# Performance work log

Measured on AMD Instinct MI355X. Metric: run time of the kernel, lower is better.

The kernel has to match this reference:

```python
import jax, jax.numpy as jnp
import numpy as np

EPS = 1e-6

def _layernorm(x):
    mu = jnp.mean(x, axis=-1, keepdims=True)
    var = jnp.mean(jnp.square(x - mu), axis=-1, keepdims=True)
    return (x - mu) / jnp.sqrt(var + EPS)

def setup_inputs() -> dict:
    key = jax.random.key(0)
    ks = jax.random.split(key, 12)
    B, N, C = 4, 1024, 1024
    H = 16
    Dff = 4 * C
    s = 0.02
    x = jax.random.normal(ks[0], (B, N, C), dtype=jnp.float32)
    mask = jax.random.randint(ks[1], (N, N), 0, 2) > 0  # True = attend
    wq = jax.random.normal(ks[2], (C, C), dtype=jnp.float32) * s
    bq = jnp.zeros((C,), dtype=jnp.float32)
    wkv = jax.random.normal(ks[3], (C, 2 * C), dtype=jnp.float32) * s
    bkv = jnp.zeros((2 * C,), dtype=jnp.float32)
    wo = jax.random.normal(ks[4], (C, C), dtype=jnp.float32) * s
    bo = jnp.zeros((C,), dtype=jnp.float32)
    w1 = jax.random.normal(ks[5], (C, Dff), dtype=jnp.float32) * s
    b1 = jnp.zeros((Dff,), dtype=jnp.float32)
    w2 = jax.random.normal(ks[6], (Dff, C), dtype=jnp.float32) * s
    b2 = jnp.zeros((C,), dtype=jnp.float32)
    return {"x": x, "mask": mask, "wq": wq, "bq": bq, "wkv": wkv, "bkv": bkv,
            "wo": wo, "bo": bo, "w1": w1, "b1": b1, "w2": w2, "b2": b2}

def reference(x, mask, wq, bq, wkv, bkv, wo, bo, w1, b1, w2, b2):
    B, N, C = x.shape
    H = 16
    d = C // H
    scale = d ** -0.5
    max_neg = -jnp.finfo(x.dtype).max
    # attn_bias: 0 where mask True, -max where False; broadcast [1,1,N,N]
    attn_bias = jnp.where(mask, jnp.asarray(0.0, x.dtype), jnp.asarray(max_neg, x.dtype))[None, None]

    # --- pre-norm attention ---
    xn = _layernorm(x)
    q = (xn @ wq + bq).reshape(B, N, H, d)
    kv = xn @ wkv + bkv
    k, v = jnp.split(kv, 2, axis=-1)
    k = k.reshape(B, N, H, d)
    v = v.reshape(B, N, H, d)
    sim = jnp.einsum('bihd,bjhd->bhij', q, k) * scale + attn_bias
    attn = jax.nn.softmax(sim, axis=-1)
    o = jnp.einsum('bhij,bjhd->bihd', attn, v).reshape(B, N, C)
    x = x + (o @ wo + bo)

    # --- pre-norm MLP with tanh-approx GELU ---
    xn = _layernorm(x)
    h = jax.nn.gelu(xn @ w1 + b1, approximate=True)
    x = x + (h @ w2 + b2)
    return x
```

## Files before the change

### kernel.cpp

```cpp
#include <hip/hip_runtime.h>
#include <hip/hip_bf16.h>

typedef short bf16x8 __attribute__((ext_vector_type(8)));
typedef float f32x4 __attribute__((ext_vector_type(4)));
typedef unsigned short u16x8 __attribute__((ext_vector_type(8)));

#define MFMA16(a,b,c) __builtin_amdgcn_mfma_f32_16x16x32_bf16((a),(b),(c),0,0,0)

__device__ inline unsigned short f32_to_bf16(float f){
  union { float f; unsigned u; } v; v.f = f;
  unsigned u = v.u;
  u += 0x7FFFu + ((u >> 16) & 1u);
  return (unsigned short)(u >> 16);
}
__device__ inline float bf16_to_f32(unsigned short u){
  union { unsigned u; float f; } v; v.u = ((unsigned)u)<<16; return v.f;
}

__device__ inline float gelu_tanh(float x){
  float x3 = x*x*x;
  float t = tanhf(0.7978845608028654f*(x + 0.044715f*x3));
  return 0.5f*x*(1.0f+t);
}

__device__ inline void gload16(const void* g, void* l){
  __builtin_amdgcn_global_load_lds(
      (const __attribute__((address_space(1))) void*)g,
      (__attribute__((address_space(3))) void*)l, 16, 0, 0);
}

__device__ inline int xcd_swz(int lin, int nwg){
  int cpx = nwg >> 3;
  return (lin & 7)*cpx + (lin >> 3);
}

__global__ void detect_mask_kernel(const unsigned* __restrict__ m, int* __restrict__ flag){
  __shared__ int s;
  if (threadIdx.x == 0) s = 0;
  __syncthreads();
  unsigned w = m[threadIdx.x];
  if (w > 1u) atomicOr(&s, 1);
  __syncthreads();
  if (threadIdx.x == 0) *flag = s;
}

__global__ __launch_bounds__(256) void mask_bias_kernel(
    const void* __restrict__ mask, const int* __restrict__ flag,
    unsigned short* __restrict__ biasr){
  __shared__ float mt[16][64];
  int qg = blockIdx.x, jt = blockIdx.y;
  int t = threadIdx.x;
  int fl = *flag;
  int jc = jt*64 + (t&63);
  #pragma unroll
  for (int k2=0;k2<4;k2++){
    int qr = qg*16 + (t>>6) + k2*4;
    bool a = fl ? (((const unsigned char*)mask)[(size_t)qr*1024 + jc] != 0)
                : (((const int*)mask)[(size_t)qr*1024 + jc] != 0);
    mt[(t>>6)+k2*4][t&63] = a ? -23.083120654223414f : -1e30f;
  }
  __syncthreads();
  ushort4 ob;
  unsigned short tmp[4];
  #pragma unroll
  for (int u=0;u<4;u++){
    int p = t*4+u;
    int e = p&15, lane = p>>4;
    int i = e>>2, jj = e&3;
    int ln2 = lane&15, g2 = lane>>4;
    tmp[u] = f32_to_bf16(mt[g2*4+i][jj*16+ln2]);
  }
  ob.x=tmp[0]; ob.y=tmp[1]; ob.z=tmp[2]; ob.w=tmp[3];
  *(ushort4*)&biasr[((size_t)(qg*16+jt)*64)*16 + t*4] = ob;
}

__global__ __launch_bounds__(256) void transpose_cvt_kernel(
    const float* __restrict__ W, unsigned short* __restrict__ WT, int K, int N){
  __shared__ float tile[32][37];
  int n0 = blockIdx.x*32, k0 = blockIdx.y*32;
  int r = threadIdx.x>>3, c4 = threadIdx.x&7;
  float4 v = *(const float4*)&W[(size_t)(k0+r)*N + n0 + c4*4];
  tile[r][c4*4+0]=v.x; tile[r][c4*4+1]=v.y; tile[r][c4*4+2]=v.z; tile[r][c4*4+3]=v.w;
  __syncthreads();
  ushort4 o;
  o.x = f32_to_bf16(tile[c4*4+0][r]);
  o.y = f32_to_bf16(tile[c4*4+1][r]);
  o.z = f32_to_bf16(tile[c4*4+2][r]);
  o.w = f32_to_bf16(tile[c4*4+3][r]);
  *(ushort4*)&WT[(size_t)(n0+r)*K + k0 + c4*4] = o;
}

__global__ __launch_bounds__(256) void vtrans_kernel(
    const unsigned short* __restrict__ qkv, unsigned short* __restrict__ vt){
  __shared__ unsigned short t[32][33];
  int b = blockIdx.z;
  int n0 = blockIdx.x*32, d0 = blockIdx.y*32;
  int tx = threadIdx.x & 31, ty = threadIdx.x >> 5;
  #pragma unroll
  for (int r=0;r<4;r++)
    t[ty+8*r][tx] = qkv[(size_t)(b*1024 + n0+ty+8*r)*3072 + 2048 + d0+tx];
  __syncthreads();
  #pragma unroll
  for (int r=0;r<4;r++)
    vt[((size_t)b<<20) + (size_t)(d0+ty+8*r)*1024 + n0+tx] = t[tx][ty+8*r];
}

__global__ void bias_concat_kernel(const float* __restrict__ bq,
                                   const float* __restrict__ bkv,
                                   float* __restrict__ dst){
  int i = blockIdx.x*256 + threadIdx.x;
  if (i < 3072) dst[i] = (i < 1024) ? bq[i] : bkv[i-1024];
}

__global__ __launch_bounds__(256) void ln_kernel(const float* __restrict__ x,
                                                 unsigned short* __restrict__ xn){
  const int C = 1024;
  size_t row = blockIdx.x;
  float4 v = reinterpret_cast<const float4*>(x + row*C)[threadIdx.x];
  float s = v.x+v.y+v.z+v.w;
  float q = v.x*v.x+v.y*v.y+v.z*v.z+v.w*v.w;
  #pragma unroll
  for (int off=32; off; off>>=1){ s += __shfl_xor(s,off); q += __shfl_xor(q,off); }
  __shared__ float sm[8];
  int wv = threadIdx.x>>6, ln = threadIdx.x&63;
  if (ln==0){ sm[wv]=s; sm[4+wv]=q; }
  __syncthreads();
  float S = sm[0]+sm[1]+sm[2]+sm[3];
  float Q = sm[4]+sm[5]+sm[6]+sm[7];
  float mu  = S*(1.0f/1024.0f);
  float var = Q*(1.0f/1024.0f) - mu*mu;
  float inv = rsqrtf(var + 1e-6f);
  ushort4 o;
  o.x = f32_to_bf16((v.x-mu)*inv);
  o.y = f32_to_bf16((v.y-mu)*inv);
  o.z = f32_to_bf16((v.z-mu)*inv);
  o.w = f32_to_bf16((v.w-mu)*inv);
  reinterpret_cast<ushort4*>(xn + row*C)[threadIdx.x] = o;
}

template<int EPI>
__global__ __launch_bounds__(64) void gemm1w_kernel(
    const unsigned short* __restrict__ A,
    const unsigned short* __restrict__ BT,
    const float* __restrict__ bias,
    const float* __restrict__ resid,
    void* __restrict__ Cout,
    int M, int N, int K)
{
  __shared__ __align__(16) unsigned short lds[4][4096];
  int lane = threadIdx.x;
  int nbx = gridDim.x;
  int lin = blockIdx.y*nbx + blockIdx.x;
  int w = xcd_swz(lin, nbx*gridDim.y);
  int m0 = (w/nbx)*64;
  int n0 = (w%nbx)*64;
  int ln = lane&15, g = lane>>4;

  int srow = lane>>2;
  int scol = (((lane&3) ^ ((lane>>3)&3)))*8;
  const unsigned short* gA = A  + (size_t)(m0+srow)*K + scol;
  const unsigned short* gB = BT + (size_t)(n0+srow)*K + scol;

  f32x4 acc[4][4] = {};
  int nt = K/32;
  const int rdsw = (g ^ ((ln>>1)&3))*8;

  auto STAGE = [&](int t, int buf){
    int ko = t*32;
    #pragma unroll
    for (int j=0;j<4;j++)
      gload16(gA + (size_t)(j*16)*K + ko, &lds[buf][j*512]);
    #pragma unroll
    for (int j=0;j<4;j++)
      gload16(gB + (size_t)(j*16)*K + ko, &lds[buf][2048 + j*512]);
  };

  STAGE(0,0); STAGE(1,1); STAGE(2,2);

  for (int t=0; t<nt; ++t){
    int rem = nt-1-t;
    if (rem >= 2)      asm volatile("s_waitcnt vmcnt(16)" ::: "memory");
    else if (rem == 1) asm volatile("s_waitcnt vmcnt(8)" ::: "memory");
    else               asm volatile("s_waitcnt vmcnt(0)" ::: "memory");
    const unsigned short* lb = lds[t&3];
    bf16x8 a[4], b[4];
    #pragma unroll
    for (int mi=0;mi<4;mi++)
      a[mi] = *(const bf16x8*)(lb + (mi*16+ln)*32 + rdsw);
    #pragma unroll
    for (int ni=0;ni<4;ni++)
      b[ni] = *(const bf16x8*)(lb + 2048 + (ni*16+ln)*32 + rdsw);
    #pragma unroll
    for (int mi=0;mi<4;mi++)
      #pragma unroll
      for (int ni=0;ni<4;ni++)
        acc[mi][ni] = MFMA16(a[mi], b[ni], acc[mi][ni]);
    asm volatile("s_waitcnt lgkmcnt(0)" ::: "memory");
    if (t+3 < nt) STAGE(t+3, (t+3)&3);
  }

  #pragma unroll
  for (int mi=0;mi<4;mi++){
    int r0 = m0 + mi*16 + g*4;
    #pragma unroll
    for (int ni=0;ni<4;ni++){
      int c = n0 + ni*16 + ln;
      float bs = bias[c];
      f32x4 cc = acc[mi][ni];
      #pragma unroll
      for (int i=0;i<4;i++){
        int r = r0 + i;
        float v = cc[i] + bs;
        if (EPI == 1){
          v += resid[(size_t)r*N + c];
          ((float*)Cout)[(size_t)r*N + c] = v;
        } else if (EPI == 2){
          ((unsigned short*)Cout)[(size_t)r*N + c] = f32_to_bf16(gelu_tanh(v));
        } else {
          ((unsigned short*)Cout)[(size_t)r*N + c] = f32_to_bf16(v);
        }
      }
    }
  }
}

template<int EPI>
__global__ __launch_bounds__(512) void gemm8_kernel(
    const unsigned short* __restrict__ A,
    const unsigned short* __restrict__ BT,
    const float* __restrict__ bias,
    void* __restrict__ Cout,
    int M, int N, int K)
{
  extern __shared__ __align__(16) char smem[];
  const int tid = threadIdx.x, wave = tid>>6, lane = tid&63;
  const int ln = lane&15, g = lane>>4;
  const int wm = wave>>2, wn = wave&3;
  const int nbx = gridDim.x;
  const int lin = blockIdx.y*nbx + blockIdx.x;
  const int wsw = xcd_swz(lin, nbx*gridDim.y);
  const int m0 = (wsw/nbx)*256, n0 = (wsw%nbx)*256;
  const int NT = K>>6;
  const int axor = (g*16) ^ (((ln>>2)&3)<<4);

  auto STAGE = [&](int kt, int h){
    const bool isB = h&1; const int kh = h>>1;
    const unsigned short* src = isB ? BT : A;
    const int base0 = isB ? n0 : m0;
    char* region = smem + (isB?65536:0) + (kt&1)*32768 + kh*16384;
    #pragma unroll
    for (int r=0;r<2;r++){
      int idx = r*512 + tid;
      int row = idx>>2;
      int col = kt*64 + kh*32 + ((((idx&3)*16) ^ (((row>>2)&3)<<4))>>1);
      gload16(src + (size_t)(base0+row)*K + col,
              region + (r*512 + wave*64)*16);
    }
  };

  STAGE(0,0); STAGE(0,1); STAGE(0,2); STAGE(0,3);
  STAGE(1,0); STAGE(1,1); STAGE(1,2);
  asm volatile("s_waitcnt vmcnt(6)" ::: "memory");
  __builtin_amdgcn_s_barrier();
  __builtin_amdgcn_sched_barrier(0);

  f32x4 acc[8][4] = {};
  bf16x8 a[8], b[2];

  for (int t=0; t<NT; ++t){
    const int cur = t&1;
    char* Ac0 = smem + cur*32768;
    char* Ac1 = Ac0 + 16384;
    char* Bc0 = smem + 65536 + cur*32768;
    char* Bc1 = Bc0 + 16384;
    #pragma unroll
    for (int mi=0;mi<8;mi++)
      a[mi] = *(const bf16x8*)(Ac0 + (wm*128+mi*16+ln)*64 + axor);
    b[0] = *(const bf16x8*)(Bc0 + (wn*64+ 0+ln)*64 + axor);
    b[1] = *(const bf16x8*)(Bc0 + (wn*64+16+ln)*64 + axor);
    if (t+1 < NT) STAGE(t+1,3);
    __builtin_amdgcn_s_barrier();
    __builtin_amdgcn_s_setprio(1);
    #pragma unroll
    for (int mi=0;mi<8;mi++){
      acc[mi][0] = MFMA16(a[mi], b[0], acc[mi][0]);
      acc[mi][1] = MFMA16(a[mi], b[1], acc[mi][1]);
    }
    __builtin_amdgcn_s_setprio(0);
    __builtin_amdgcn_s_barrier();
    b[0] = *(const bf16x8*)(Bc0 + (wn*64+32+ln)*64 + axor);
    b[1] = *(const bf16x8*)(Bc0 + (wn*64+48+ln)*64 + axor);
    if (t+2 < NT) STAGE(t+2,0);
    __builtin_amdgcn_s_barrier();
    __builtin_amdgcn_s_setprio(1);
    #pragma unroll
    for (int mi=0;mi<8;mi++){
      acc[mi][2] = MFMA16(a[mi], b[0], acc[mi][2]);
      acc[mi][3] = MFMA16(a[mi], b[1], acc[mi][3]);
    }
    __builtin_amdgcn_s_setprio(0);
    __builtin_amdgcn_s_barrier();
    #pragma unroll
    for (int mi=0;mi<8;mi++)
      a[mi] = *(const bf16x8*)(Ac1 + (wm*128+mi*16+ln)*64 + axor);
    b[0] = *(const bf16x8*)(Bc1 + (wn*64+ 0+ln)*64 + axor);
    b[1] = *(const bf16x8*)(Bc1 + (wn*64+16+ln)*64 + axor);
    if (t+2 < NT) STAGE(t+2,1);
    __builtin_amdgcn_s_barrier();
    __builtin_amdgcn_s_setprio(1);
    #pragma unroll
    for (int mi=0;mi<8;mi++){
      acc[mi][0] = MFMA16(a[mi], b[0], acc[mi][0]);
      acc[mi][1] = MFMA16(a[mi], b[1], acc[mi][1]);
    }
    __builtin_amdgcn_s_setprio(0);
    __builtin_amdgcn_s_barrier();
    b[0] = *(const bf16x8*)(Bc1 + (wn*64+32+ln)*64 + axor);
    b[1] = *(const bf16x8*)(Bc1 + (wn*64+48+ln)*64 + axor);
    if (t+2 < NT) STAGE(t+2,2);
    __builtin_amdgcn_s_barrier();
    __builtin_amdgcn_s_setprio(1);
    #pragma unroll
    for (int mi=0;mi<8;mi++){
      acc[mi][2] = MFMA16(a[mi], b[0], acc[mi][2]);
      acc[mi][3] = MFMA16(a[mi], b[1], acc[mi][3]);
    }
    __builtin_amdgcn_s_setprio(0);
    if (t+2 < NT) asm volatile("s_waitcnt vmcnt(6)" ::: "memory");
    else          asm volatile("s_waitcnt vmcnt(0)" ::: "memory");
    __builtin_amdgcn_s_barrier();
    __builtin_amdgcn_sched_barrier(0);
  }

  #pragma unroll
  for (int mi=0;mi<8;mi++){
    int r0 = m0 + wm*128 + mi*16 + g*4;
    #pragma unroll
    for (int nj=0;nj<4;nj++){
      int c = n0 + wn*64 + nj*16 + ln;
      float bs = bias[c];
      f32x4 cc = acc[mi][nj];
      #pragma unroll
      for (int i=0;i<4;i++){
        int r = r0 + i;
        float v = cc[i] + bs;
        if (EPI == 2){
          ((unsigned short*)Cout)[(size_t)r*N + c] = f32_to_bf16(gelu_tanh(v));
        } else {
          ((unsigned short*)Cout)[(size_t)r*N + c] = f32_to_bf16(v);
        }
      }
    }
  }
}

__global__ __launch_bounds__(256,6) void attn_kernel(
    const unsigned short* __restrict__ qkv,
    const unsigned short* __restrict__ vt,
    const unsigned short* __restrict__ biasr,
    unsigned short* __restrict__ pn,
    float* __restrict__ lsumg)
{
  const int N = 1024, NK = 3072;
  const float SCL = 0.18033688011112042f;
  __shared__ __align__(16) unsigned short lK[64*64];
  __shared__ __align__(16) unsigned short lV[64*64];
  __shared__ __align__(16) unsigned short plds[4][16][72];
  int bh = blockIdx.x, qt = blockIdx.y, sp = blockIdx.z;
  int b = bh>>4, h = bh&15;
  int tid = threadIdx.x, wave = tid>>6, lane = tid&63;
  int ln = lane&15, g = lane>>4;
  size_t base = (size_t)b*N;
  int q_local = qt*64 + wave*16;

  const unsigned short* qptr = qkv + (base + q_local + ln)*NK + h*64;
  bf16x8 aq0 = *(const bf16x8*)(qptr + g*8);
  bf16x8 aq1 = *(const bf16x8*)(qptr + 32 + g*8);

  int r0s = tid>>3,        c0 = (tid&7) ^ (r0s&7);
  int r1s = 32 + (tid>>3), c1 = (tid&7) ^ (r1s&7);
  const unsigned short* kg0 = qkv + (base + r0s)*NK + 1024 + h*64 + c0*8;
  const unsigned short* kg1 = qkv + (base + r1s)*NK + 1024 + h*64 + c1*8;
  const unsigned short* vg0 = vt + ((size_t)b<<20) + (size_t)(h*64 + r0s)*N + c0*8;
  const unsigned short* vg1 = vt + ((size_t)b<<20) + (size_t)(h*64 + r1s)*N + c1*8;
  char* lKd0 = (char*)lK + (wave*64)*16;
  char* lKd1 = (char*)lK + (256 + wave*64)*16;
  char* lVd0 = (char*)lV + (wave*64)*16;
  char* lVd1 = (char*)lV + (256 + wave*64)*16;

  const unsigned short* brp = biasr +
      (((size_t)(qt*4 + wave)*16)*64 + lane)*16;

  f32x4 oacc[4] = {};
  float lsum[4] = {0.f,0.f,0.f,0.f};
  const int xl = (ln&7);

  for (int t=0; t<8; ++t){
    int j0 = sp*512 + t*64;
    __syncthreads();
    gload16(kg0 + (size_t)j0*NK, lKd0);
    gload16(kg1 + (size_t)j0*NK, lKd1);
    gload16(vg0 + j0, lVd0);
    gload16(vg1 + j0, lVd1);
    int jt = j0>>6;
    bf16x8 bb0 = *(const bf16x8*)(brp + (size_t)jt*1024);
    bf16x8 bb1 = *(const bf16x8*)(brp + (size_t)jt*1024 + 8);
    asm volatile("s_waitcnt vmcnt(0)" ::: "memory");
    __builtin_amdgcn_s_barrier();

    f32x4 s[4];
    #pragma unroll
    for (int jj=0;jj<4;jj++){
      int row = jj*16+ln;
      bf16x8 k0 = *(const bf16x8*)((const char*)lK + row*128 + ((g^xl)<<4));
      bf16x8 k1 = *(const bf16x8*)((const char*)lK + row*128 + (((g+4)^xl)<<4));
      s[jj] = (f32x4){};
      s[jj] = MFMA16(aq0, k0, s[jj]);
      s[jj] = MFMA16(aq1, k1, s[jj]);
    }
    #pragma unroll
    for (int i=0;i<4;i++){
      #pragma unroll
      for (int jj=0;jj<4;jj++){
        int e = i*4+jj;
        unsigned short bu = (e<8) ? (unsigned short)bb0[e] : (unsigned short)bb1[e-8];
        float ev = exp2f(fmaf(s[jj][i], SCL, bf16_to_f32(bu)));
        lsum[i] += ev;
        plds[wave][4*g+i][jj*16+ln] = f32_to_bf16(ev);
      }
    }
    asm volatile("s_waitcnt lgkmcnt(0)" ::: "memory");
    __builtin_amdgcn_sched_barrier(0);
    bf16x8 p0 = *(const bf16x8*)&plds[wave][ln][g*8];
    bf16x8 p1 = *(const bf16x8*)&plds[wave][ln][32 + g*8];
    #pragma unroll
    for (int nd=0;nd<4;nd++){
      int row = nd*16+ln;
      bf16x8 v0 = *(const bf16x8*)((const char*)lV + row*128 + ((g^xl)<<4));
      bf16x8 v1 = *(const bf16x8*)((const char*)lV + row*128 + (((g+4)^xl)<<4));
      oacc[nd] = MFMA16(p0, v0, oacc[nd]);
      oacc[nd] = MFMA16(p1, v1, oacc[nd]);
    }
  }

  #pragma unroll
  for (int i=0;i<4;i++){
    float l = lsum[i];
    l += __shfl_xor(l,1); l += __shfl_xor(l,2);
    l += __shfl_xor(l,4); l += __shfl_xor(l,8);
    if (ln == 0)
      lsumg[((size_t)sp<<16) + (size_t)(base + q_local + 4*g + i)*16 + h] = l;
  }
  #pragma unroll
  for (int nd=0;nd<4;nd++){
    #pragma unroll
    for (int i=0;i<4;i++){
      int qr = q_local + 4*g + i;
      pn[((size_t)sp<<22) + (base+qr)*1024 + h*64 + nd*16 + ln] = f32_to_bf16(oacc[nd][i]);
    }
  }
}

__global__ __launch_bounds__(256) void attn_reduce_kernel(
    const unsigned short* __restrict__ pn,
    const float* __restrict__ lsumg,
    unsigned short* __restrict__ o)
{
  size_t idx = ((size_t)blockIdx.x*256 + threadIdx.x)*8;
  int r = (int)(idx>>10);
  int h = (int)((idx&1023)>>6);
  float inv = 1.0f/(lsumg[(size_t)r*16+h] + lsumg[(1u<<16) + (size_t)r*16+h]);
  u16x8 p0 = *(const u16x8*)(pn + idx);
  u16x8 p1 = *(const u16x8*)(pn + (1u<<22) + idx);
  u16x8 res;
  #pragma unroll
  for (int e=0;e<8;e++)
    res[e] = f32_to_bf16((bf16_to_f32((unsigned short)p0[e]) +
                          bf16_to_f32((unsigned short)p1[e]))*inv);
  *(u16x8*)(o + idx) = res;
}

extern "C" void kernel_launch(void* const* d_in, const int* in_sizes, int n_in,
                              void* d_out, int out_size, void* d_ws, size_t ws_size,
                              hipStream_t stream)
{
  (void)in_sizes; (void)n_in; (void)out_size; (void)ws_size;
  const float* x   = (const float*)d_in[0];
  const void*  mask= d_in[1];
  const float* wq  = (const float*)d_in[2];
  const float* bq  = (const float*)d_in[3];
  const float* wkv = (const float*)d_in[4];
  const float* bkv = (const float*)d_in[5];
  const float* wo  = (const float*)d_in[6];
  const float* bo  = (const float*)d_in[7];
  const float* w1  = (const float*)d_in[8];
  const float* b1  = (const float*)d_in[9];
  const float* w2  = (const float*)d_in[10];
  const float* b2  = (const float*)d_in[11];
  float* out = (float*)d_out;

  char* ws = (char*)d_ws;
  size_t off = 0;
  auto alloc = [&](size_t bytes){ size_t o = off; off += (bytes + 255) & ~(size_t)255; return o; };
  unsigned short* WqkvT = (unsigned short*)(ws + alloc(3072u*1024u*2));
  unsigned short* WoT   = (unsigned short*)(ws + alloc(1024u*1024u*2));
  unsigned short* W1T   = (unsigned short*)(ws + alloc(4096u*1024u*2));
  unsigned short* W2T   = (unsigned short*)(ws + alloc(1024u*4096u*2));
  float*          BIASQ = (float*)(ws + alloc(3072u*4));
  int*            FLAG  = (int*)(ws + alloc(256));
  float*          LSUM  = (float*)(ws + alloc(2u*4096u*16u*4));
  unsigned short* BIASR = (unsigned short*)(ws + alloc(64u*16u*64u*16u*2));
  unsigned short* XN    = (unsigned short*)(ws + alloc(4096u*1024u*2));
  float*          X1    = (float*)(ws + alloc(4096u*1024u*4));
  unsigned short* QKV   = (unsigned short*)(ws + alloc(4096u*4096u*2));
  unsigned short* VT    = QKV + (size_t)4096u*3072u;
  unsigned short* PN    = (unsigned short*)X1;

  hipFuncSetAttribute(reinterpret_cast<const void*>(&gemm8_kernel<0>),
                      hipFuncAttributeMaxDynamicSharedMemorySize, 131072);
  hipFuncSetAttribute(reinterpret_cast<const void*>(&gemm8_kernel<2>),
                      hipFuncAttributeMaxDynamicSharedMemorySize, 131072);

  transpose_cvt_kernel<<<dim3(32,32),  256, 0, stream>>>(wq,  WqkvT,               1024, 1024);
  transpose_cvt_kernel<<<dim3(64,32),  256, 0, stream>>>(wkv, WqkvT + 1024u*1024u, 1024, 2048);
  transpose_cvt_kernel<<<dim3(32,32),  256, 0, stream>>>(wo,  WoT,                 1024, 1024);
  transpose_cvt_kernel<<<dim3(128,32), 256, 0, stream>>>(w1,  W1T,                 1024, 4096);
  transpose_cvt_kernel<<<dim3(32,128), 256, 0, stream>>>(w2,  W2T,                 4096, 1024);
  bias_concat_kernel<<<12, 256, 0, stream>>>(bq, bkv, BIASQ);
  detect_mask_kernel<<<1, 256, 0, stream>>>((const unsigned*)mask, FLAG);
  mask_bias_kernel<<<dim3(64,16), 256, 0, stream>>>(mask, FLAG, BIASR);

  ln_kernel<<<4096, 256, 0, stream>>>(x, XN);
  gemm8_kernel<0><<<dim3(12,16), 512, 131072, stream>>>(XN, WqkvT, BIASQ, QKV, 4096, 3072, 1024);
  vtrans_kernel<<<dim3(32,32,4), 256, 0, stream>>>(QKV, VT);
  attn_kernel<<<dim3(64,16,2), 256, 0, stream>>>(QKV, VT, BIASR, PN, LSUM);
  attn_reduce_kernel<<<2048, 256, 0, stream>>>(PN, LSUM, XN);
  gemm1w_kernel<1><<<dim3(16,64), 64, 0, stream>>>(XN, WoT, bo, x, X1, 4096, 1024, 1024);
  ln_kernel<<<4096, 256, 0, stream>>>(X1, XN);
  gemm8_kernel<2><<<dim3(16,16), 512, 131072, stream>>>(XN, W1T, b1, QKV, 4096, 4096, 1024);
  gemm1w_kernel<1><<<dim3(16,64), 64, 0, stream>>>(QKV, W2T, b2, X1, out, 4096, 1024, 4096);
}
```

Baseline: 264.7 us.

## Run MLP down-projection with split-K 256x256 MFMA GEMM plus reduction

The second MLP GEMM (K=4096) moves from the small-tile single-wave gemm1w kernel to the 256x256 gemm8 kernel, split four ways along K to give 256 blocks. Split 0 writes bias plus residual plus its partial in fp32. The other splits write bf16 partial planes into workspace buffers that are dead at that point (XN, W1T, the start of the workspace). A new elementwise kernel then adds the three planes into the output. This aims to use larger tiles with more data reuse, at the cost of extra partial-sum traffic, one more launch, and some precision loss from storing partials in bf16.

After: 283.7 us. 1.07x slower.

```diff
diff --git a/kernel.cpp b/kernel.cpp
--- a/kernel.cpp
+++ b/kernel.cpp
@@ -224,13 +224,18 @@
   }
 }
 
-template<int EPI>
+template<int MODE>
 __global__ __launch_bounds__(512) void gemm8_kernel(
     const unsigned short* __restrict__ A,
     const unsigned short* __restrict__ BT,
     const float* __restrict__ bias,
-    void* __restrict__ Cout,
-    int M, int N, int K)
+    const float* __restrict__ resid,
+    float* __restrict__ fout,
+    unsigned short* __restrict__ p1,
+    unsigned short* __restrict__ p2,
+    unsigned short* __restrict__ p3,
+    unsigned short* __restrict__ bf16out,
+    int M, int N, int K, int Ksp)
 {
   extern __shared__ __align__(16) char smem[];
   const int tid = threadIdx.x, wave = tid>>6, lane = tid&63;
@@ -240,7 +245,8 @@
   const int lin = blockIdx.y*nbx + blockIdx.x;
   const int wsw = xcd_swz(lin, nbx*gridDim.y);
   const int m0 = (wsw/nbx)*256, n0 = (wsw%nbx)*256;
-  const int NT = K>>6;
+  const int NT = Ksp>>6;
+  const int kbase = (MODE==3) ? blockIdx.z*Ksp : 0;
   const int axor = (g*16) ^ (((ln>>2)&3)<<4);
 
   auto STAGE = [&](int kt, int h){
@@ -252,7 +258,7 @@
     for (int r=0;r<2;r++){
       int idx = r*512 + tid;
       int row = idx>>2;
-      int col = kt*64 + kh*32 + ((((idx&3)*16) ^ (((row>>2)&3)<<4))>>1);
+      int col = kbase + kt*64 + kh*32 + ((((idx&3)*16) ^ (((row>>2)&3)<<4))>>1);
       gload16(src + (size_t)(base0+row)*K + col,
               region + (r*512 + wave*64)*16);
     }
@@ -331,6 +337,10 @@
     __builtin_amdgcn_s_barrier();
     __builtin_amdgcn_sched_barrier(0);
   }
+
+  unsigned short* plane = nullptr;
+  if (MODE == 3 && blockIdx.z > 0)
+    plane = (blockIdx.z==1) ? p1 : ((blockIdx.z==2) ? p2 : p3);
 
   #pragma unroll
   for (int mi=0;mi<8;mi++){
@@ -343,15 +353,43 @@
       #pragma unroll
       for (int i=0;i<4;i++){
         int r = r0 + i;
-        float v = cc[i] + bs;
-        if (EPI == 2){
-          ((unsigned short*)Cout)[(size_t)r*N + c] = f32_to_bf16(gelu_tanh(v));
+        if (MODE == 3){
+          if (blockIdx.z == 0){
+            fout[(size_t)r*N + c] = cc[i] + bs + resid[(size_t)r*N + c];
+          } else {
+            plane[(size_t)r*N + c] = f32_to_bf16(cc[i]);
+          }
+        } else if (MODE == 2){
+          bf16out[(size_t)r*N + c] = f32_to_bf16(gelu_tanh(cc[i] + bs));
         } else {
-          ((unsigned short*)Cout)[(size_t)r*N + c] = f32_to_bf16(v);
+          bf16out[(size_t)r*N + c] = f32_to_bf16(cc[i] + bs);
         }
       }
     }
   }
+}
+
+__global__ __launch_bounds__(256) void mlp2_reduce_kernel(
+    float* __restrict__ out,
+    const unsigned short* __restrict__ p1,
+    const unsigned short* __restrict__ p2,
+    const unsigned short* __restrict__ p3)
+{
+  size_t i8 = ((size_t)blockIdx.x*256 + threadIdx.x)*8;
+  float4 o0 = *(const float4*)(out + i8);
+  float4 o1 = *(const float4*)(out + i8 + 4);
+  u16x8 a = *(const u16x8*)(p1 + i8);
+  u16x8 b = *(const u16x8*)(p2 + i8);
+  u16x8 c = *(const u16x8*)(p3 + i8);
+  float r[8];
+  #pragma unroll
+  for (int e=0;e<8;e++)
+    r[e] = bf16_to_f32((unsigned short)a[e]) + bf16_to_f32((unsigned short)b[e])
+         + bf16_to_f32((unsigned short)c[e]);
+  o0.x+=r[0]; o0.y+=r[1]; o0.z+=r[2]; o0.w+=r[3];
+  o1.x+=r[4]; o1.y+=r[5]; o1.z+=r[6]; o1.w+=r[7];
+  *(float4*)(out + i8) = o0;
+  *(float4*)(out + i8 + 4) = o1;
 }
 
 __global__ __launch_bounds__(256,6) void attn_kernel(
@@ -515,10 +553,15 @@
   unsigned short* QKV   = (unsigned short*)(ws + alloc(4096u*4096u*2));
   unsigned short* VT    = QKV + (size_t)4096u*3072u;
   unsigned short* PN    = (unsigned short*)X1;
+  unsigned short* PL1 = XN;
+  unsigned short* PL2 = W1T;
+  unsigned short* PL3 = (unsigned short*)ws;
 
   hipFuncSetAttribute(reinterpret_cast<const void*>(&gemm8_kernel<0>),
                       hipFuncAttributeMaxDynamicSharedMemorySize, 131072);
   hipFuncSetAttribute(reinterpret_cast<const void*>(&gemm8_kernel<2>),
+                      hipFuncAttributeMaxDynamicSharedMemorySize, 131072);
+  hipFuncSetAttribute(reinterpret_cast<const void*>(&gemm8_kernel<3>),
                       hipFuncAttributeMaxDynamicSharedMemorySize, 131072);
 
   transpose_cvt_kernel<<<dim3(32,32),  256, 0, stream>>>(wq,  WqkvT,               1024, 1024);
@@ -531,12 +574,19 @@
   mask_bias_kernel<<<dim3(64,16), 256, 0, stream>>>(mask, FLAG, BIASR);
 
   ln_kernel<<<4096, 256, 0, stream>>>(x, XN);
-  gemm8_kernel<0><<<dim3(12,16), 512, 131072, stream>>>(XN, WqkvT, BIASQ, QKV, 4096, 3072, 1024);
+  gemm8_kernel<0><<<dim3(12,16), 512, 131072, stream>>>(
+      XN, WqkvT, BIASQ, nullptr, nullptr, nullptr, nullptr, nullptr, QKV,
+      4096, 3072, 1024, 1024);
   vtrans_kernel<<<dim3(32,32,4), 256, 0, stream>>>(QKV, VT);
   attn_kernel<<<dim3(64,16,2), 256, 0, stream>>>(QKV, VT, BIASR, PN, LSUM);
   attn_reduce_kernel<<<2048, 256, 0, stream>>>(PN, LSUM, XN);
   gemm1w_kernel<1><<<dim3(16,64), 64, 0, stream>>>(XN, WoT, bo, x, X1, 4096, 1024, 1024);
   ln_kernel<<<4096, 256, 0, stream>>>(X1, XN);
-  gemm8_kernel<2><<<dim3(16,16), 512, 131072, stream>>>(XN, W1T, b1, QKV, 4096, 4096, 1024);
-  gemm1w_kernel<1><<<dim3(16,64), 64, 0, stream>>>(QKV, W2T, b2, X1, out, 4096, 1024, 4096);
-}
+  gemm8_kernel<2><<<dim3(16,16), 512, 131072, stream>>>(
+      XN, W1T, b1, nullptr, nullptr, nullptr, nullptr, nullptr, QKV,
+      4096, 4096, 1024, 1024);
+  gemm8_kernel<3><<<dim3(4,16,4), 512, 131072, stream>>>(
+      QKV, W2T, b2, X1, out, PL1, PL2, PL3, nullptr,
+      4096, 1024, 4096, 1024);
+  mlp2_reduce_kernel<<<2048, 256, 0, stream>>>(out, PL1, PL2, PL3);
+}
```

## Split-K the MLP down-projection GEMM and reduce partials in a separate kernel

Applied to the files above, without the earlier changes.

The final w2 GEMM (K=4096) now runs as a two-way split-K over a 3D grid. The z=0 slice writes bias plus residual plus its partial in fp32 to the output, and the z=1 slice writes its partial as bf16 into a scratch plane that reuses the XN buffer. A new reduce kernel adds that plane into the output. This is meant to double the block count and shorten the per-block K loop for better occupancy, at the cost of an extra pass over memory and bf16 rounding of half the sum. The single-wave GEMM's LDS pipeline also drops from 4 to 2 buffers (prefetch depth 3 to 2), which frees LDS per block for more resident blocks but hides less load latency.

After: 287.1 us. 1.08x slower.

```diff
diff --git a/kernel.cpp b/kernel.cpp
--- a/kernel.cpp
+++ b/kernel.cpp
@@ -138,31 +138,33 @@
   reinterpret_cast<ushort4*>(xn + row*C)[threadIdx.x] = o;
 }
 
-template<int EPI>
+template<int MODE>
 __global__ __launch_bounds__(64) void gemm1w_kernel(
     const unsigned short* __restrict__ A,
     const unsigned short* __restrict__ BT,
     const float* __restrict__ bias,
     const float* __restrict__ resid,
     void* __restrict__ Cout,
-    int M, int N, int K)
+    unsigned short* __restrict__ plane,
+    int M, int N, int K, int Ksp)
 {
-  __shared__ __align__(16) unsigned short lds[4][4096];
+  __shared__ __align__(16) unsigned short lds[2][4096];
   int lane = threadIdx.x;
   int nbx = gridDim.x;
   int lin = blockIdx.y*nbx + blockIdx.x;
   int w = xcd_swz(lin, nbx*gridDim.y);
   int m0 = (w/nbx)*64;
   int n0 = (w%nbx)*64;
+  int kbase = (MODE==3) ? blockIdx.z*Ksp : 0;
   int ln = lane&15, g = lane>>4;
 
   int srow = lane>>2;
   int scol = (((lane&3) ^ ((lane>>3)&3)))*8;
-  const unsigned short* gA = A  + (size_t)(m0+srow)*K + scol;
-  const unsigned short* gB = BT + (size_t)(n0+srow)*K + scol;
+  const unsigned short* gA = A  + (size_t)(m0+srow)*K + kbase + scol;
+  const unsigned short* gB = BT + (size_t)(n0+srow)*K + kbase + scol;
 
   f32x4 acc[4][4] = {};
-  int nt = K/32;
+  int nt = Ksp/32;
   const int rdsw = (g ^ ((ln>>1)&3))*8;
 
   auto STAGE = [&](int t, int buf){
@@ -175,14 +177,12 @@
       gload16(gB + (size_t)(j*16)*K + ko, &lds[buf][2048 + j*512]);
   };
 
-  STAGE(0,0); STAGE(1,1); STAGE(2,2);
+  STAGE(0,0); STAGE(1,1);
 
   for (int t=0; t<nt; ++t){
-    int rem = nt-1-t;
-    if (rem >= 2)      asm volatile("s_waitcnt vmcnt(16)" ::: "memory");
-    else if (rem == 1) asm volatile("s_waitcnt vmcnt(8)" ::: "memory");
-    else               asm volatile("s_waitcnt vmcnt(0)" ::: "memory");
-    const unsigned short* lb = lds[t&3];
+    if (t+1 < nt) asm volatile("s_waitcnt vmcnt(8)" ::: "memory");
+    else          asm volatile("s_waitcnt vmcnt(0)" ::: "memory");
+    const unsigned short* lb = lds[t&1];
     bf16x8 a[4], b[4];
     #pragma unroll
     for (int mi=0;mi<4;mi++)
@@ -196,7 +196,7 @@
       for (int ni=0;ni<4;ni++)
         acc[mi][ni] = MFMA16(a[mi], b[ni], acc[mi][ni]);
     asm volatile("s_waitcnt lgkmcnt(0)" ::: "memory");
-    if (t+3 < nt) STAGE(t+3, (t+3)&3);
+    if (t+2 < nt) STAGE(t+2, t&1);
   }
 
   #pragma unroll
@@ -205,23 +205,40 @@
     #pragma unroll
     for (int ni=0;ni<4;ni++){
       int c = n0 + ni*16 + ln;
-      float bs = bias[c];
       f32x4 cc = acc[mi][ni];
       #pragma unroll
       for (int i=0;i<4;i++){
         int r = r0 + i;
-        float v = cc[i] + bs;
-        if (EPI == 1){
-          v += resid[(size_t)r*N + c];
-          ((float*)Cout)[(size_t)r*N + c] = v;
-        } else if (EPI == 2){
-          ((unsigned short*)Cout)[(size_t)r*N + c] = f32_to_bf16(gelu_tanh(v));
+        if (MODE == 3){
+          if (blockIdx.z == 0)
+            ((float*)Cout)[(size_t)r*N + c] = cc[i] + bias[c] + resid[(size_t)r*N + c];
+          else
+            plane[(size_t)r*N + c] = f32_to_bf16(cc[i]);
         } else {
-          ((unsigned short*)Cout)[(size_t)r*N + c] = f32_to_bf16(v);
+          ((float*)Cout)[(size_t)r*N + c] = cc[i] + bias[c] + resid[(size_t)r*N + c];
         }
       }
     }
   }
+}
+
+__global__ __launch_bounds__(256) void mlp2_reduce_kernel(
+    float* __restrict__ out, const unsigned short* __restrict__ p1)
+{
+  size_t i8 = ((size_t)blockIdx.x*256 + threadIdx.x)*8;
+  float4 o0 = *(const float4*)(out + i8);
+  float4 o1 = *(const float4*)(out + i8 + 4);
+  u16x8 a = *(const u16x8*)(p1 + i8);
+  o0.x += bf16_to_f32((unsigned short)a[0]);
+  o0.y += bf16_to_f32((unsigned short)a[1]);
+  o0.z += bf16_to_f32((unsigned short)a[2]);
+  o0.w += bf16_to_f32((unsigned short)a[3]);
+  o1.x += bf16_to_f32((unsigned short)a[4]);
+  o1.y += bf16_to_f32((unsigned short)a[5]);
+  o1.z += bf16_to_f32((unsigned short)a[6]);
+  o1.w += bf16_to_f32((unsigned short)a[7]);
+  *(float4*)(out + i8) = o0;
+  *(float4*)(out + i8 + 4) = o1;
 }
 
 template<int EPI>
@@ -515,6 +532,7 @@
   unsigned short* QKV   = (unsigned short*)(ws + alloc(4096u*4096u*2));
   unsigned short* VT    = QKV + (size_t)4096u*3072u;
   unsigned short* PN    = (unsigned short*)X1;
+  unsigned short* PL1   = XN;
 
   hipFuncSetAttribute(reinterpret_cast<const void*>(&gemm8_kernel<0>),
                       hipFuncAttributeMaxDynamicSharedMemorySize, 131072);
@@ -535,8 +553,11 @@
   vtrans_kernel<<<dim3(32,32,4), 256, 0, stream>>>(QKV, VT);
   attn_kernel<<<dim3(64,16,2), 256, 0, stream>>>(QKV, VT, BIASR, PN, LSUM);
   attn_reduce_kernel<<<2048, 256, 0, stream>>>(PN, LSUM, XN);
-  gemm1w_kernel<1><<<dim3(16,64), 64, 0, stream>>>(XN, WoT, bo, x, X1, 4096, 1024, 1024);
+  gemm1w_kernel<1><<<dim3(16,64), 64, 0, stream>>>(
+      XN, WoT, bo, x, X1, nullptr, 4096, 1024, 1024, 1024);
   ln_kernel<<<4096, 256, 0, stream>>>(X1, XN);
   gemm8_kernel<2><<<dim3(16,16), 512, 131072, stream>>>(XN, W1T, b1, QKV, 4096, 4096, 1024);
-  gemm1w_kernel<1><<<dim3(16,64), 64, 0, stream>>>(QKV, W2T, b2, X1, out, 4096, 1024, 4096);
-}
+  gemm1w_kernel<3><<<dim3(16,64,2), 64, 0, stream>>>(
+      QKV, W2T, b2, X1, out, PL1, 4096, 1024, 4096, 2048);
+  mlp2_reduce_kernel<<<2048, 256, 0, stream>>>(out, PL1);
+}
```

## Replace single-wave 64x64 GEMM with 4-wave 128x128 tile GEMM sharing LDS

Applied to the files above, without the earlier changes.

The single-wave 64x64 tile kernel used for the output projection and MLP down-projection becomes a 256-thread kernel. Four waves each compute a 64x64 quadrant of a 128x128 tile and share cooperatively loaded A/B slices in a 3-stage LDS ring. This halves global reads per output element and improves operand reuse. In exchange it adds block barriers each k-step and cuts the grid to 256 blocks, which may leave CUs underused on a large GPU.

Result: faster. 249.0 us (-5.9%).

```diff
diff --git a/kernel.cpp b/kernel.cpp
--- a/kernel.cpp
+++ b/kernel.cpp
@@ -139,7 +139,7 @@
 }
 
 template<int EPI>
-__global__ __launch_bounds__(64) void gemm1w_kernel(
+__global__ __launch_bounds__(256) void gemm128_kernel(
     const unsigned short* __restrict__ A,
     const unsigned short* __restrict__ BT,
     const float* __restrict__ bias,
@@ -147,19 +147,25 @@
     void* __restrict__ Cout,
     int M, int N, int K)
 {
-  __shared__ __align__(16) unsigned short lds[4][4096];
-  int lane = threadIdx.x;
+  __shared__ __align__(16) unsigned short lds[3][8192];
+  int tid = threadIdx.x, wave = tid>>6, lane = tid&63;
   int nbx = gridDim.x;
   int lin = blockIdx.y*nbx + blockIdx.x;
   int w = xcd_swz(lin, nbx*gridDim.y);
-  int m0 = (w/nbx)*64;
-  int n0 = (w%nbx)*64;
+  int m0 = (w/nbx)*128, n0 = (w%nbx)*128;
   int ln = lane&15, g = lane>>4;
-
-  int srow = lane>>2;
-  int scol = (((lane&3) ^ ((lane>>3)&3)))*8;
-  const unsigned short* gA = A  + (size_t)(m0+srow)*K + scol;
-  const unsigned short* gB = BT + (size_t)(n0+srow)*K + scol;
+  int wm = wave>>1, wn = wave&1;
+
+  const unsigned short* sA[2];
+  const unsigned short* sB[2];
+  #pragma unroll
+  for (int p=0;p<2;p++){
+    int idx = p*256 + tid;
+    int row = idx>>2, c = idx&3;
+    int ch = c ^ ((row>>1)&3);
+    sA[p] = A  + (size_t)(m0+row)*K + ch*8;
+    sB[p] = BT + (size_t)(n0+row)*K + ch*8;
+  }
 
   f32x4 acc[4][4] = {};
   int nt = K/32;
@@ -168,43 +174,49 @@
   auto STAGE = [&](int t, int buf){
     int ko = t*32;
     #pragma unroll
-    for (int j=0;j<4;j++)
-      gload16(gA + (size_t)(j*16)*K + ko, &lds[buf][j*512]);
-    #pragma unroll
-    for (int j=0;j<4;j++)
-      gload16(gB + (size_t)(j*16)*K + ko, &lds[buf][2048 + j*512]);
+    for (int p=0;p<2;p++)
+      gload16(sA[p]+ko, (char*)&lds[buf][0]    + (p*256 + wave*64)*16);
+    #pragma unroll
+    for (int p=0;p<2;p++)
+      gload16(sB[p]+ko, (char*)&lds[buf][4096] + (p*256 + wave*64)*16);
   };
 
   STAGE(0,0); STAGE(1,1); STAGE(2,2);
 
+  int cb = 0;
   for (int t=0; t<nt; ++t){
     int rem = nt-1-t;
-    if (rem >= 2)      asm volatile("s_waitcnt vmcnt(16)" ::: "memory");
-    else if (rem == 1) asm volatile("s_waitcnt vmcnt(8)" ::: "memory");
+    if (rem >= 2)      asm volatile("s_waitcnt vmcnt(8)" ::: "memory");
+    else if (rem == 1) asm volatile("s_waitcnt vmcnt(4)" ::: "memory");
     else               asm volatile("s_waitcnt vmcnt(0)" ::: "memory");
-    const unsigned short* lb = lds[t&3];
+    __builtin_amdgcn_s_barrier();
+
+    const unsigned short* lb = lds[cb];
     bf16x8 a[4], b[4];
     #pragma unroll
     for (int mi=0;mi<4;mi++)
-      a[mi] = *(const bf16x8*)(lb + (mi*16+ln)*32 + rdsw);
+      a[mi] = *(const bf16x8*)(lb + (wm*64+mi*16+ln)*32 + rdsw);
     #pragma unroll
     for (int ni=0;ni<4;ni++)
-      b[ni] = *(const bf16x8*)(lb + 2048 + (ni*16+ln)*32 + rdsw);
+      b[ni] = *(const bf16x8*)(lb + 4096 + (wn*64+ni*16+ln)*32 + rdsw);
     #pragma unroll
     for (int mi=0;mi<4;mi++)
       #pragma unroll
       for (int ni=0;ni<4;ni++)
         acc[mi][ni] = MFMA16(a[mi], b[ni], acc[mi][ni]);
+
     asm volatile("s_waitcnt lgkmcnt(0)" ::: "memory");
-    if (t+3 < nt) STAGE(t+3, (t+3)&3);
+    __builtin_amdgcn_s_barrier();
+    if (t+3 < nt) STAGE(t+3, cb);
+    cb = (cb==2) ? 0 : cb+1;
   }
 
   #pragma unroll
   for (int mi=0;mi<4;mi++){
-    int r0 = m0 + mi*16 + g*4;
+    int r0 = m0 + wm*64 + mi*16 + g*4;
     #pragma unroll
     for (int ni=0;ni<4;ni++){
-      int c = n0 + ni*16 + ln;
+      int c = n0 + wn*64 + ni*16 + ln;
       float bs = bias[c];
       f32x4 cc = acc[mi][ni];
       #pragma unroll
@@ -535,8 +547,8 @@
   vtrans_kernel<<<dim3(32,32,4), 256, 0, stream>>>(QKV, VT);
   attn_kernel<<<dim3(64,16,2), 256, 0, stream>>>(QKV, VT, BIASR, PN, LSUM);
   attn_reduce_kernel<<<2048, 256, 0, stream>>>(PN, LSUM, XN);
-  gemm1w_kernel<1><<<dim3(16,64), 64, 0, stream>>>(XN, WoT, bo, x, X1, 4096, 1024, 1024);
+  gemm128_kernel<1><<<dim3(8,32), 256, 0, stream>>>(XN, WoT, bo, x, X1, 4096, 1024, 1024);
   ln_kernel<<<4096, 256, 0, stream>>>(X1, XN);
   gemm8_kernel<2><<<dim3(16,16), 512, 131072, stream>>>(XN, W1T, b1, QKV, 4096, 4096, 1024);
-  gemm1w_kernel<1><<<dim3(16,64), 64, 0, stream>>>(QKV, W2T, b2, X1, out, 4096, 1024, 4096);
-}
+  gemm128_kernel<1><<<dim3(8,32), 256, 0, stream>>>(QKV, W2T, b2, X1, out, 4096, 1024, 4096);
+}
```
